# Kernel optimization log

Hardware: AMD Instinct MI355X
Metric: run time of the kernel (lower is better)

## Reference

```python
import jax, jax.numpy as jnp
import numpy as np

D = 192          # d_model
H = 8            # n_heads
DH = D // H      # d_head = 24
DFF = 2 * D      # FeedForward hidden = d_model*2
SIZES = [384 + 8 * i for i in range(32)]   # ragged segment lengths
TOTAL = sum(SIZES)                          # 16256
EPS = 1e-5

# static ragged -> padded index maps (numpy, baked at trace time)
_sz = np.asarray(SIZES)
B = len(_sz)
MAXN = int(_sz.max())
SEG = np.repeat(np.arange(B), _sz)                      # [TOTAL] segment id
POS = np.concatenate([np.arange(s) for s in _sz])       # [TOTAL] position in segment
PADMASK = np.ones((B, MAXN), dtype=bool)                # True = padding (key_padding_mask)
PADMASK[SEG, POS] = False


def _layernorm(x, gamma, beta):
    mu = jnp.mean(x, axis=-1, keepdims=True)
    var = jnp.var(x, axis=-1, keepdims=True)
    return (x - mu) * jax.lax.rsqrt(var + EPS) * gamma + beta


def setup_inputs() -> dict:
    key = jax.random.key(0)
    ks = jax.random.split(key, 8)
    w = lambda k, shape: jax.random.normal(k, shape, jnp.float32) * 0.02
    return {
        "x": jax.random.normal(ks[0], (TOTAL, D), jnp.float32),
        "sizes": jnp.asarray(SIZES, jnp.int32),
        "Wqkv": w(ks[1], (3 * D, D)), "bqkv": jnp.zeros((3 * D,), jnp.float32),
        "Wo": w(ks[2], (D, D)),       "bo": jnp.zeros((D,), jnp.float32),
        "Wg": w(ks[3], (D, 2 * D)),   "bg": jnp.zeros((D,), jnp.float32),
        "gamma1": jnp.ones((D,), jnp.float32), "beta1": jnp.zeros((D,), jnp.float32),
        "W1": w(ks[4], (DFF, D)),     "b1": jnp.zeros((DFF,), jnp.float32),
        "W2": w(ks[5], (D, DFF)),     "b2": jnp.zeros((D,), jnp.float32),
        "gamma2": jnp.ones((D,), jnp.float32), "beta2": jnp.zeros((D,), jnp.float32),
    }


def reference(x, sizes, Wqkv, bqkv, Wo, bo, Wg, bg, gamma1, beta1,
              W1, b1, W2, b2, gamma2, beta2):
    # --- pad_by_sizes (vectorized scatter, static index maps) ---
    pad = jnp.zeros((B, MAXN, D), x.dtype).at[SEG, POS].set(x)   # [B, MAXN, D]

    # --- nn.MultiheadAttention (batch_first, key_padding_mask) ---
    qkv = pad @ Wqkv.T + bqkv                                    # [B, MAXN, 3D]
    q, k, v = jnp.split(qkv, 3, axis=-1)
    def heads(t):  # [B, MAXN, D] -> [B, H, MAXN, DH]
        return t.reshape(B, MAXN, H, DH).transpose(0, 2, 1, 3)
    q, k, v = heads(q), heads(k), heads(v)
    scores = jnp.einsum("bhqd,bhkd->bhqk", q, k) / np.sqrt(DH)   # [B, H, MAXN, MAXN]
    scores = jnp.where(PADMASK[:, None, None, :], jnp.float32(-1e9), scores)
    attn = jax.nn.softmax(scores, axis=-1)
    o = jnp.einsum("bhqk,bhkd->bhqd", attn, v)                   # [B, H, MAXN, DH]
    o = o.transpose(0, 2, 1, 3).reshape(B, MAXN, D)
    out = o @ Wo.T + bo                                          # [B, MAXN, D]

    # --- gather back to ragged; gate/norm/ff are per-token, so the torch
    # per-segment loop is equivalent to one vectorized pass over all tokens ---
    out_flat = out[SEG, POS]                                     # [TOTAL, D]
    g = jax.nn.sigmoid(jnp.concatenate([out_flat, x], axis=-1) @ Wg.T + bg)
    h = g * out_flat + (1.0 - g) * x                             # GatedResidual
    h = _layernorm(h, gamma1, beta1)                             # self.norm
    y = jax.nn.silu(h @ W1.T + b1) @ W2.T + b2                   # FeedForward.net
    return _layernorm(h + y, gamma2, beta2)                      # residual + norm
```

## Files before the change

kernel.cpp:

```cpp
#include <hip/hip_runtime.h>
#include <math.h>

#define D_      192
#define H_      8
#define DH_     24
#define NSEG    32
#define TOTAL_  16256
static constexpr float LN_EPS = 1e-5f;
static constexpr float SCALE  = 0.20412414523193154f;
static constexpr float SC_L2E = 0.29446679331797463f;

typedef float  f32x4  __attribute__((ext_vector_type(4)));
typedef short  bf16x8 __attribute__((ext_vector_type(8)));
typedef unsigned short u16x4 __attribute__((ext_vector_type(4)));
typedef unsigned int   u32x4 __attribute__((ext_vector_type(4)));

__device__ __forceinline__ unsigned short f2b(float f) {
    union { float f; unsigned u; } v; v.f = f;
    unsigned r = v.u + 0x7FFFu + ((v.u >> 16) & 1u);
    return (unsigned short)(r >> 16);
}
__device__ __forceinline__ unsigned f2b_u32(float f) {
    union { float f; unsigned u; } v; v.f = f;
    return (v.u + 0x8000u) >> 16;
}
__device__ __forceinline__ unsigned short f2b_fast(float f) {
    union { float f; unsigned u; } v; v.f = f;
    return (unsigned short)((v.u + 0x8000u) >> 16);
}
__device__ __forceinline__ float b2f(unsigned short h) {
    union { unsigned u; float f; } v; v.u = (unsigned)h << 16; return v.f;
}
__device__ __forceinline__ float fexp2(float x) {
#if __has_builtin(__builtin_amdgcn_exp2f)
    return __builtin_amdgcn_exp2f(x);
#else
    return exp2f(x);
#endif
}

#define NXE 3121152
__global__ __launch_bounds__(256)
void conv_all(const float* __restrict__ x,
              const float* __restrict__ w0, const float* __restrict__ w1,
              const float* __restrict__ w2, const float* __restrict__ w3,
              const float* __restrict__ w4,
              unsigned short* __restrict__ xb, unsigned short* __restrict__ wb)
{
    int i = (blockIdx.x * 256 + threadIdx.x) * 4;
    const float* src; unsigned short* dst; int off;
    if (i < NXE) { src = x; dst = xb; off = 0; }
    else {
        int j = i - NXE; dst = wb;
        if      (j < 110592) { src = w0; off = 0; }
        else if (j < 147456) { src = w1; off = 110592; }
        else if (j < 221184) { src = w2; off = 147456; }
        else if (j < 294912) { src = w3; off = 221184; }
        else                 { src = w4; off = 294912; }
        i = j;
    }
    float4 v = *(const float4*)&src[i - off];
    u16x4 o = { f2b(v.x), f2b(v.y), f2b(v.z), f2b(v.w) };
    *(u16x4*)&dst[i] = o;
}

template<int KF, int MR, int OUT_BF16>
__global__ __launch_bounds__(256)
void gemm_lds(const unsigned short* __restrict__ Ain,
              const unsigned short* __restrict__ Wb,
              const float* __restrict__ bias,
              void* __restrict__ Cout, int N)
{
    constexpr int KSW = KF * 32 + 8;
    __shared__ unsigned short Wp[64 * KSW];

    const int tid = threadIdx.x;
    const int wv  = tid >> 6;
    const int l   = tid & 63;
    const int m0  = blockIdx.x * (64 * MR) + wv * (16 * MR);
    const int n0  = blockIdx.y * 64;
    const int rl  = l & 15;
    const int kc  = (l >> 4) * 8;

    bf16x8 afrag[MR][KF];
    #pragma unroll
    for (int h = 0; h < MR; ++h)
        #pragma unroll
        for (int kk = 0; kk < KF; ++kk)
            afrag[h][kk] = *(const bf16x8*)&Ain[(size_t)(m0 + h * 16 + rl) * (KF * 32) + kk * 32 + kc];

    #pragma unroll
    for (int i = 0; i < KF; ++i) {
        int u = i * 256 + tid;
        int row = u / (KF * 4), c = u % (KF * 4);
        *(bf16x8*)&Wp[row * KSW + c * 8] = *(const bf16x8*)&Wb[(size_t)(n0 + row) * (KF * 32) + c * 8];
    }
    __syncthreads();

    f32x4 acc[MR][4] = {};
    #pragma unroll
    for (int kk = 0; kk < KF; ++kk) {
        #pragma unroll
        for (int nf = 0; nf < 4; ++nf) {
            bf16x8 b = *(const bf16x8*)&Wp[(nf * 16 + rl) * KSW + kk * 32 + kc];
            #pragma unroll
            for (int h = 0; h < MR; ++h)
                acc[h][nf] = __builtin_amdgcn_mfma_f32_16x16x32_bf16(afrag[h][kk], b, acc[h][nf], 0, 0, 0);
        }
    }

    #pragma unroll
    for (int h = 0; h < MR; ++h) {
        #pragma unroll
        for (int nf = 0; nf < 4; ++nf) {
            const int c = n0 + nf * 16 + rl;
            const float bz = bias[c];
            #pragma unroll
            for (int q = 0; q < 4; ++q) {
                const int r = m0 + h * 16 + (l >> 4) * 4 + q;
                float v = acc[h][nf][q] + bz;
                if (OUT_BF16) ((unsigned short*)Cout)[(size_t)r * N + c] = f2b(v);
                else          ((float*)Cout)[(size_t)r * N + c] = v;
            }
        }
    }
}

__global__ __launch_bounds__(256, 2)
void wo_gate_ln1(const unsigned short* __restrict__ o_b,
                 const unsigned short* __restrict__ xb,
                 const unsigned short* __restrict__ wo_b,
                 const unsigned short* __restrict__ wg_b,
                 const float* __restrict__ bo, const float* __restrict__ bg,
                 const float* __restrict__ gamma1, const float* __restrict__ beta1,
                 unsigned short* __restrict__ h1b)
{
    constexpr int WS = 200;
    __shared__ unsigned short Wp[96 * WS];
    __shared__ unsigned short Al[64 * WS];

    const int tid = threadIdx.x;
    const int wv  = tid >> 6;
    const int l   = tid & 63;
    const int rl  = l & 15;
    const int g   = l >> 4;
    const int kc  = g * 8;
    const int m0  = blockIdx.x * 64 + wv * 16;

    bf16x8 afA[6];
    #pragma unroll
    for (int kk = 0; kk < 6; ++kk)
        afA[kk] = *(const bf16x8*)&o_b[(size_t)(m0 + rl) * 192 + kk * 32 + kc];

    f32x4 accA[12] = {};
    #pragma unroll
    for (int sub = 0; sub < 2; ++sub) {
        __syncthreads();
        #pragma unroll
        for (int i = 0; i < 9; ++i) {
            int u = i * 256 + tid;
            int row = u / 24, c = u % 24;
            *(bf16x8*)&Wp[row * WS + c * 8] = *(const bf16x8*)&wo_b[(size_t)(sub * 96 + row) * 192 + c * 8];
        }
        __syncthreads();
        #pragma unroll
        for (int kk = 0; kk < 6; ++kk)
            #pragma unroll
            for (int nf2 = 0; nf2 < 6; ++nf2) {
                bf16x8 b = *(const bf16x8*)&Wp[(nf2 * 16 + rl) * WS + kk * 32 + kc];
                accA[sub * 6 + nf2] = __builtin_amdgcn_mfma_f32_16x16x32_bf16(afA[kk], b, accA[sub * 6 + nf2], 0, 0, 0);
            }
    }

    float att[12][4];
    #pragma unroll
    for (int nf = 0; nf < 12; ++nf) {
        const int cnf = (nf / 6) * 96 + (nf % 6) * 16 + rl;
        const float bz = bo[cnf];
        #pragma unroll
        for (int q = 0; q < 4; ++q) {
            att[nf][q] = accA[nf][q] + bz;
            Al[(wv * 16 + g * 4 + q) * WS + cnf] = f2b(att[nf][q]);
        }
    }

    bf16x8 afX[6];
    #pragma unroll
    for (int kk = 0; kk < 6; ++kk)
        afX[kk] = *(const bf16x8*)&xb[(size_t)(m0 + rl) * 192 + kk * 32 + kc];

    f32x4 accB[12] = {};
    #pragma unroll
    for (int kb = 0; kb < 2; ++kb)
        #pragma unroll
        for (int sub = 0; sub < 2; ++sub) {
            __syncthreads();
            #pragma unroll
            for (int i = 0; i < 9; ++i) {
                int u = i * 256 + tid;
                int row = u / 24, c = u % 24;
                *(bf16x8*)&Wp[row * WS + c * 8] = *(const bf16x8*)&wg_b[(size_t)(sub * 96 + row) * 384 + kb * 192 + c * 8];
            }
            __syncthreads();
            #pragma unroll
            for (int kk = 0; kk < 6; ++kk) {
                bf16x8 a = (kb == 0) ? *(const bf16x8*)&Al[(wv * 16 + rl) * WS + kk * 32 + kc]
                                     : afX[kk];
                #pragma unroll
                for (int nf2 = 0; nf2 < 6; ++nf2) {
                    bf16x8 b = *(const bf16x8*)&Wp[(nf2 * 16 + rl) * WS + kk * 32 + kc];
                    accB[sub * 6 + nf2] = __builtin_amdgcn_mfma_f32_16x16x32_bf16(a, b, accB[sub * 6 + nf2], 0, 0, 0);
                }
            }
        }

    float bz[12], gam[12], bet[12];
    #pragma unroll
    for (int nf = 0; nf < 12; ++nf) {
        const int cnf = (nf / 6) * 96 + (nf % 6) * 16 + rl;
        bz[nf]  = bg[cnf];
        gam[nf] = gamma1[cnf];
        bet[nf] = beta1[cnf];
    }
    #pragma unroll
    for (int q = 0; q < 4; ++q) {
        const int r = m0 + g * 4 + q;
        const size_t rb = (size_t)r * 192;
        float h[12];
        float s = 0.f;
        #pragma unroll
        for (int nf = 0; nf < 12; ++nf) {
            const int cnf = (nf / 6) * 96 + (nf % 6) * 16 + rl;
            float v  = accB[nf][q] + bz[nf];
            float gt = 1.f / (1.f + __expf(-v));
            h[nf] = gt * att[nf][q] + (1.f - gt) * b2f(xb[rb + cnf]);
            s += h[nf];
        }
        s += __shfl_xor(s, 1); s += __shfl_xor(s, 2);
        s += __shfl_xor(s, 4); s += __shfl_xor(s, 8);
        const float mu = s * (1.f / 192.f);
        float sq = 0.f;
        #pragma unroll
        for (int nf = 0; nf < 12; ++nf) { float d = h[nf] - mu; sq += d * d; }
        sq += __shfl_xor(sq, 1); sq += __shfl_xor(sq, 2);
        sq += __shfl_xor(sq, 4); sq += __shfl_xor(sq, 8);
        const float rstd = rsqrtf(sq * (1.f / 192.f) + LN_EPS);
        #pragma unroll
        for (int nf = 0; nf < 12; ++nf) {
            const int cnf = (nf / 6) * 96 + (nf % 6) * 16 + rl;
            h1b[rb + cnf] = f2b((h[nf] - mu) * rstd * gam[nf] + bet[nf]);
        }
    }
}

__global__ __launch_bounds__(256, 2)
void ffn_ln2(const unsigned short* __restrict__ h1b,
             const unsigned short* __restrict__ w1_b,
             const unsigned short* __restrict__ w2_b,
             const float* __restrict__ b1, const float* __restrict__ b2,
             const float* __restrict__ gamma2, const float* __restrict__ beta2,
             float* __restrict__ out)
{
    constexpr int WS = 200;
    __shared__ unsigned short Wp[96 * WS];
    __shared__ unsigned short Fl[64 * WS];

    const int tid = threadIdx.x;
    const int wv  = tid >> 6;
    const int l   = tid & 63;
    const int rl  = l & 15;
    const int g   = l >> 4;
    const int kc  = g * 8;
    const int m0  = blockIdx.x * 64 + wv * 16;

    bf16x8 afC[6];
    #pragma unroll
    for (int kk = 0; kk < 6; ++kk)
        afC[kk] = *(const bf16x8*)&h1b[(size_t)(m0 + rl) * 192 + kk * 32 + kc];

    f32x4 accD[12] = {};
    #pragma unroll
    for (int ch = 0; ch < 2; ++ch) {
        f32x4 accC[12] = {};
        #pragma unroll
        for (int sub = 0; sub < 2; ++sub) {
            __syncthreads();
            #pragma unroll
            for (int i = 0; i < 9; ++i) {
                int u = i * 256 + tid;
                int row = u / 24, c = u % 24;
                *(bf16x8*)&Wp[row * WS + c * 8] = *(const bf16x8*)&w1_b[(size_t)(ch * 192 + sub * 96 + row) * 192 + c * 8];
            }
            __syncthreads();
            #pragma unroll
            for (int kk = 0; kk < 6; ++kk)
                #pragma unroll
                for (int nf2 = 0; nf2 < 6; ++nf2) {
                    bf16x8 b = *(const bf16x8*)&Wp[(nf2 * 16 + rl) * WS + kk * 32 + kc];
                    accC[sub * 6 + nf2] = __builtin_amdgcn_mfma_f32_16x16x32_bf16(afC[kk], b, accC[sub * 6 + nf2], 0, 0, 0);
                }
        }
        #pragma unroll
        for (int nf = 0; nf < 12; ++nf) {
            const int colc = (nf / 6) * 96 + (nf % 6) * 16 + rl;
            const float bz1 = b1[ch * 192 + colc];
            #pragma unroll
            for (int q = 0; q < 4; ++q) {
                float v = accC[nf][q] + bz1;
                float s = 1.f / (1.f + __expf(-v));
                Fl[(wv * 16 + g * 4 + q) * WS + colc] = f2b(v * s);
            }
        }
        #pragma unroll
        for (int sub = 0; sub < 2; ++sub) {
            __syncthreads();
            #pragma unroll
            for (int i = 0; i < 9; ++i) {
                int u = i * 256 + tid;
                int row = u / 24, c = u % 24;
                *(bf16x8*)&Wp[row * WS + c * 8] = *(const bf16x8*)&w2_b[(size_t)(sub * 96 + row) * 384 + ch * 192 + c * 8];
            }
            __syncthreads();
            #pragma unroll
            for (int kk = 0; kk < 6; ++kk) {
                bf16x8 a = *(const bf16x8*)&Fl[(wv * 16 + rl) * WS + kk * 32 + kc];
                #pragma unroll
                for (int nf2 = 0; nf2 < 6; ++nf2) {
                    bf16x8 b = *(const bf16x8*)&Wp[(nf2 * 16 + rl) * WS + kk * 32 + kc];
                    accD[sub * 6 + nf2] = __builtin_amdgcn_mfma_f32_16x16x32_bf16(a, b, accD[sub * 6 + nf2], 0, 0, 0);
                }
            }
        }
    }

    float bz[12], gam[12], bet[12];
    #pragma unroll
    for (int nf = 0; nf < 12; ++nf) {
        const int cnf = (nf / 6) * 96 + (nf % 6) * 16 + rl;
        bz[nf]  = b2[cnf];
        gam[nf] = gamma2[cnf];
        bet[nf] = beta2[cnf];
    }
    #pragma unroll
    for (int q = 0; q < 4; ++q) {
        const int r = m0 + g * 4 + q;
        const size_t rb = (size_t)r * 192;
        float h[12];
        float s = 0.f;
        #pragma unroll
        for (int nf = 0; nf < 12; ++nf) {
            const int cnf = (nf / 6) * 96 + (nf % 6) * 16 + rl;
            h[nf] = b2f(h1b[rb + cnf]) + accD[nf][q] + bz[nf];
            s += h[nf];
        }
        s += __shfl_xor(s, 1); s += __shfl_xor(s, 2);
        s += __shfl_xor(s, 4); s += __shfl_xor(s, 8);
        const float mu = s * (1.f / 192.f);
        float sq = 0.f;
        #pragma unroll
        for (int nf = 0; nf < 12; ++nf) { float d = h[nf] - mu; sq += d * d; }
        sq += __shfl_xor(sq, 1); sq += __shfl_xor(sq, 2);
        sq += __shfl_xor(sq, 4); sq += __shfl_xor(sq, 8);
        const float rstd = rsqrtf(sq * (1.f / 192.f) + LN_EPS);
        #pragma unroll
        for (int nf = 0; nf < 12; ++nf) {
            const int cnf = (nf / 6) * 96 + (nf % 6) * 16 + rl;
            out[rb + cnf] = (h[nf] - mu) * rstd * gam[nf] + bet[nf];
        }
    }
}

#define KSTR 40
#define VSTR 72

__global__ __launch_bounds__(256)
void attn_mfma(const unsigned short* __restrict__ qkv, unsigned short* __restrict__ o)
{
    const int w    = blockIdx.x;
    const int xcd  = w & 7;
    const int slot = w >> 3;
    const int seg  = xcd + 8 * (slot / 40);
    const int inr  = slot % 40;
    const int head = inr / 5;
    const int q0   = (inr % 5) * 128;

    const int n    = 384 + 8 * seg;
    const int base = 384 * seg + 4 * seg * (seg - 1);
    if (q0 >= n) return;

    __shared__ unsigned short Ks[2][64 * KSTR];
    __shared__ unsigned short Vt[2][32 * VSTR];

    const int tid = threadIdx.x;
    const int wv  = tid >> 6;
    const int l   = tid & 63;
    const int lq  = l & 15;
    const int g   = l >> 4;

    if (tid < 64) {
        *(uint4*)&Ks[0][tid * KSTR + 24] = make_uint4(0, 0, 0, 0);
        *(uint4*)&Ks[1][tid * KSTR + 24] = make_uint4(0, 0, 0, 0);
    }
    for (int t4 = tid; t4 < 144; t4 += 256) {
        *(unsigned long long*)&Vt[0][24 * VSTR + t4 * 4] = 0ull;
        *(unsigned long long*)&Vt[1][24 * VSTR + t4 * 4] = 0ull;
    }

    int   qrow[2];
    bf16x8 qfrag[2];
    #pragma unroll
    for (int qf = 0; qf < 2; ++qf) {
        qrow[qf] = q0 + wv * 32 + qf * 16 + lq;
        const int qtok = base + (qrow[qf] < n ? qrow[qf] : n - 1);
        bf16x8 qz = {};
        if (g < 3) qz = *(const bf16x8*)&qkv[(size_t)qtok * 576 + head * 24 + g * 8];
        qfrag[qf] = qz;
    }

    const int sj  = tid & 63;
    const int sc  = tid >> 6;
    const int scj = 32 * (sj >> 5) + 8 * ((sj >> 2) & 3) + 4 * ((sj >> 4) & 1) + (sj & 3);

    bf16x8 kreg = {}, vreg = {};
    if (tid < 192) {
        int jr = sj; if (jr >= n) jr = n - 1;
        const unsigned short* rp = &qkv[(size_t)(base + jr) * 576 + head * 24 + sc * 8];
        kreg = *(const bf16x8*)(rp + 192);
        vreg = *(const bf16x8*)(rp + 384);
        *(bf16x8*)&Ks[0][sj * KSTR + sc * 8] = kreg;
        #pragma unroll
        for (int e = 0; e < 8; ++e)
            Vt[0][(sc * 8 + e) * VSTR + scj] = ((const unsigned short*)&vreg)[e];
    }

    float lsum[2] = {0.f, 0.f};
    f32x4 oacc[2][2] = {};

    const int nt = (n + 63) >> 6;
    int cur = 0;
    for (int t = 0; t < nt; ++t) {
        __syncthreads();
        const int j0 = t * 64;
        const bool pf = (t + 1 < nt) && (tid < 192);
        if (pf) {
            int jr = j0 + 64 + sj; if (jr >= n) jr = n - 1;
            const unsigned short* rp = &qkv[(size_t)(base + jr) * 576 + head * 24 + sc * 8];
            kreg = *(const bf16x8*)(rp + 192);
            vreg = *(const bf16x8*)(rp + 384);
        }

        bf16x8 kf[4];
        #pragma unroll
        for (int ks = 0; ks < 4; ++ks)
            kf[ks] = *(const bf16x8*)&Ks[cur][(ks * 16 + lq) * KSTR + g * 8];

        const int rem = n - j0;
        bf16x8 pfr[2][2];
        #pragma unroll
        for (int qf = 0; qf < 2; ++qf) {
            f32x4 sacc[4] = {};
            #pragma unroll
            for (int ks = 0; ks < 4; ++ks)
                sacc[ks] = __builtin_amdgcn_mfma_f32_16x16x32_bf16(kf[ks], qfrag[qf], sacc[ks], 0, 0, 0);

            float psum = 0.f;
            unsigned pw[8];
            #pragma unroll
            for (int ks = 0; ks < 4; ++ks) {
                float pv[4];
                #pragma unroll
                for (int r = 0; r < 4; ++r) {
                    float p = fexp2(sacc[ks][r] * SC_L2E);
                    if (rem < 64) { int key = ks * 16 + g * 4 + r; if (key >= rem) p = 0.f; }
                    psum += p;
                    pv[r] = p;
                }
                pw[ks * 2 + 0] = f2b_u32(pv[0]) | (f2b_u32(pv[1]) << 16);
                pw[ks * 2 + 1] = f2b_u32(pv[2]) | (f2b_u32(pv[3]) << 16);
            }
            psum += __shfl_xor(psum, 16);
            psum += __shfl_xor(psum, 32);
            lsum[qf] += psum;
            #pragma unroll
            for (int jk = 0; jk < 2; ++jk) {
                u32x4 fr = { pw[jk*4+0], pw[jk*4+1], pw[jk*4+2], pw[jk*4+3] };
                pfr[qf][jk] = *(bf16x8*)&fr;
            }
        }

        #pragma unroll
        for (int jk = 0; jk < 2; ++jk) {
            bf16x8 vf[2];
            #pragma unroll
            for (int df = 0; df < 2; ++df)
                vf[df] = *(const bf16x8*)&Vt[cur][(df * 16 + lq) * VSTR + jk * 32 + g * 8];
            #pragma unroll
            for (int qf = 0; qf < 2; ++qf)
                #pragma unroll
                for (int df = 0; df < 2; ++df)
                    oacc[qf][df] = __builtin_amdgcn_mfma_f32_16x16x32_bf16(vf[df], pfr[qf][jk], oacc[qf][df], 0, 0, 0);
        }

        if (pf) {
            *(bf16x8*)&Ks[cur ^ 1][sj * KSTR + sc * 8] = kreg;
            #pragma unroll
            for (int e = 0; e < 8; ++e)
                Vt[cur ^ 1][(sc * 8 + e) * VSTR + scj] = ((const unsigned short*)&vreg)[e];
        }
        cur ^= 1;
    }

    #pragma unroll
    for (int qf = 0; qf < 2; ++qf) {
        if (qrow[qf] < n) {
            const float rl2 = 1.f / lsum[qf];
            #pragma unroll
            for (int df = 0; df < 2; ++df) {
                const int d0 = df * 16 + g * 4;
                if (d0 < 24) {
                    u16x4 r = { f2b_fast(oacc[qf][df][0] * rl2), f2b_fast(oacc[qf][df][1] * rl2),
                                f2b_fast(oacc[qf][df][2] * rl2), f2b_fast(oacc[qf][df][3] * rl2) };
                    *(u16x4*)&o[(size_t)(base + qrow[qf]) * 192 + head * 24 + d0] = r;
                }
            }
        }
    }
}

extern "C" void kernel_launch(void* const* d_in, const int* in_sizes, int n_in,
                              void* d_out, int out_size, void* d_ws, size_t ws_size,
                              hipStream_t stream)
{
    const float* x      = (const float*)d_in[0];
    const float* Wqkv   = (const float*)d_in[2];
    const float* bqkv   = (const float*)d_in[3];
    const float* Wo     = (const float*)d_in[4];
    const float* bo     = (const float*)d_in[5];
    const float* Wg     = (const float*)d_in[6];
    const float* bg     = (const float*)d_in[7];
    const float* gamma1 = (const float*)d_in[8];
    const float* beta1  = (const float*)d_in[9];
    const float* W1     = (const float*)d_in[10];
    const float* b1     = (const float*)d_in[11];
    const float* W2     = (const float*)d_in[12];
    const float* b2     = (const float*)d_in[13];
    const float* gamma2 = (const float*)d_in[14];
    const float* beta2  = (const float*)d_in[15];
    float* out = (float*)d_out;
    float* ws  = (float*)d_ws;

    const size_t T = TOTAL_;
    unsigned short* qkv_b = (unsigned short*)ws;
    unsigned short* o_b   = (unsigned short*)(ws + 288 * T);
    unsigned short* h1b   = (unsigned short*)(ws + 384 * T);
    unsigned short* wb    = (unsigned short*)(ws + 480 * T);
    unsigned short* xb    = (unsigned short*)(ws + 492 * T);

    dim3 blk(256);

    conv_all<<<dim3(3408), blk, 0, stream>>>(x, Wqkv, Wo, Wg, W1, W2, xb, wb);
    gemm_lds<6,2,1><<<dim3(127, 9), blk, 0, stream>>>(xb, wb, bqkv, qkv_b, 576);
    attn_mfma<<<dim3(1280), blk, 0, stream>>>(qkv_b, o_b);
    wo_gate_ln1<<<dim3(254), blk, 0, stream>>>(o_b, xb, wb + 110592, wb + 147456,
                                               bo, bg, gamma1, beta1, h1b);
    ffn_ln2<<<dim3(254), blk, 0, stream>>>(h1b, wb + 221184, wb + 294912,
                                           b1, b2, gamma2, beta2, out);
}
```

Baseline: 95.90 us.

## Fuse Wo/gate/LN1 and FFN/LN2 kernels into one tail kernel

```diff
diff --git a/kernel.cpp b/kernel.cpp
--- a/kernel.cpp
+++ b/kernel.cpp
@@ -127,13 +127,17 @@
 }
 
 __global__ __launch_bounds__(256, 2)
-void wo_gate_ln1(const unsigned short* __restrict__ o_b,
-                 const unsigned short* __restrict__ xb,
-                 const unsigned short* __restrict__ wo_b,
-                 const unsigned short* __restrict__ wg_b,
-                 const float* __restrict__ bo, const float* __restrict__ bg,
-                 const float* __restrict__ gamma1, const float* __restrict__ beta1,
-                 unsigned short* __restrict__ h1b)
+void tail_fused(const unsigned short* __restrict__ o_b,
+                const unsigned short* __restrict__ xb,
+                const unsigned short* __restrict__ wo_b,
+                const unsigned short* __restrict__ wg_b,
+                const unsigned short* __restrict__ w1_b,
+                const unsigned short* __restrict__ w2_b,
+                const float* __restrict__ bo, const float* __restrict__ bg,
+                const float* __restrict__ b1, const float* __restrict__ b2,
+                const float* __restrict__ gamma1, const float* __restrict__ beta1,
+                const float* __restrict__ gamma2, const float* __restrict__ beta2,
+                float* __restrict__ out)
 {
     constexpr int WS = 200;
     __shared__ unsigned short Wp[96 * WS];
@@ -214,69 +218,58 @@
             }
         }
 
-    float bz[12], gam[12], bet[12];
+    float h1ln[12][4];
+    {
+        float bz[12], gam[12], bet[12];
+        #pragma unroll
+        for (int nf = 0; nf < 12; ++nf) {
+            const int cnf = (nf / 6) * 96 + (nf % 6) * 16 + rl;
+            bz[nf]  = bg[cnf];
+            gam[nf] = gamma1[cnf];
+            bet[nf] = beta1[cnf];
+        }
+        #pragma unroll
+        for (int q = 0; q < 4; ++q) {
+            const int r = m0 + g * 4 + q;
+            const size_t rb = (size_t)r * 192;
+            float h[12];
+            float s = 0.f;
+            #pragma unroll
+            for (int nf = 0; nf < 12; ++nf) {
+                const int cnf = (nf / 6) * 96 + (nf % 6) * 16 + rl;
+                float v  = accB[nf][q] + bz[nf];
+                float gt = 1.f / (1.f + __expf(-v));
+                h[nf] = gt * att[nf][q] + (1.f - gt) * b2f(xb[rb + cnf]);
+                s += h[nf];
+            }
+            s += __shfl_xor(s, 1); s += __shfl_xor(s, 2);
+            s += __shfl_xor(s, 4); s += __shfl_xor(s, 8);
+            const float mu = s * (1.f / 192.f);
+            float sq = 0.f;
+            #pragma unroll
+            for (int nf = 0; nf < 12; ++nf) { float d = h[nf] - mu; sq += d * d; }
+            sq += __shfl_xor(sq, 1); sq += __shfl_xor(sq, 2);
+            sq += __shfl_xor(sq, 4); sq += __shfl_xor(sq, 8);
+            const float rstd = rsqrtf(sq * (1.f / 192.f) + LN_EPS);
+            #pragma unroll
+            for (int nf = 0; nf < 12; ++nf)
+                h1ln[nf][q] = (h[nf] - mu) * rstd * gam[nf] + bet[nf];
+        }
+    }
+    __syncthreads();
     #pragma unroll
     for (int nf = 0; nf < 12; ++nf) {
         const int cnf = (nf / 6) * 96 + (nf % 6) * 16 + rl;
-        bz[nf]  = bg[cnf];
-        gam[nf] = gamma1[cnf];
-        bet[nf] = beta1[cnf];
-    }
-    #pragma unroll
-    for (int q = 0; q < 4; ++q) {
-        const int r = m0 + g * 4 + q;
-        const size_t rb = (size_t)r * 192;
-        float h[12];
-        float s = 0.f;
-        #pragma unroll
-        for (int nf = 0; nf < 12; ++nf) {
-            const int cnf = (nf / 6) * 96 + (nf % 6) * 16 + rl;
-            float v  = accB[nf][q] + bz[nf];
-            float gt = 1.f / (1.f + __expf(-v));
-            h[nf] = gt * att[nf][q] + (1.f - gt) * b2f(xb[rb + cnf]);
-            s += h[nf];
-        }
-        s += __shfl_xor(s, 1); s += __shfl_xor(s, 2);
-        s += __shfl_xor(s, 4); s += __shfl_xor(s, 8);
-        const float mu = s * (1.f / 192.f);
-        float sq = 0.f;
-        #pragma unroll
-        for (int nf = 0; nf < 12; ++nf) { float d = h[nf] - mu; sq += d * d; }
-        sq += __shfl_xor(sq, 1); sq += __shfl_xor(sq, 2);
-        sq += __shfl_xor(sq, 4); sq += __shfl_xor(sq, 8);
-        const float rstd = rsqrtf(sq * (1.f / 192.f) + LN_EPS);
-        #pragma unroll
-        for (int nf = 0; nf < 12; ++nf) {
-            const int cnf = (nf / 6) * 96 + (nf % 6) * 16 + rl;
-            h1b[rb + cnf] = f2b((h[nf] - mu) * rstd * gam[nf] + bet[nf]);
-        }
-    }
-}
-
-__global__ __launch_bounds__(256, 2)
-void ffn_ln2(const unsigned short* __restrict__ h1b,
-             const unsigned short* __restrict__ w1_b,
-             const unsigned short* __restrict__ w2_b,
-             const float* __restrict__ b1, const float* __restrict__ b2,
-             const float* __restrict__ gamma2, const float* __restrict__ beta2,
-             float* __restrict__ out)
-{
-    constexpr int WS = 200;
-    __shared__ unsigned short Wp[96 * WS];
-    __shared__ unsigned short Fl[64 * WS];
-
-    const int tid = threadIdx.x;
-    const int wv  = tid >> 6;
-    const int l   = tid & 63;
-    const int rl  = l & 15;
-    const int g   = l >> 4;
-    const int kc  = g * 8;
-    const int m0  = blockIdx.x * 64 + wv * 16;
+        #pragma unroll
+        for (int q = 0; q < 4; ++q)
+            Al[(wv * 16 + g * 4 + q) * WS + cnf] = f2b(h1ln[nf][q]);
+    }
+    __syncthreads();
 
     bf16x8 afC[6];
     #pragma unroll
     for (int kk = 0; kk < 6; ++kk)
-        afC[kk] = *(const bf16x8*)&h1b[(size_t)(m0 + rl) * 192 + kk * 32 + kc];
+        afC[kk] = *(const bf16x8*)&Al[(wv * 16 + rl) * WS + kk * 32 + kc];
 
     f32x4 accD[12] = {};
     #pragma unroll
@@ -300,6 +293,7 @@
                     accC[sub * 6 + nf2] = __builtin_amdgcn_mfma_f32_16x16x32_bf16(afC[kk], b, accC[sub * 6 + nf2], 0, 0, 0);
                 }
         }
+        __syncthreads();
         #pragma unroll
         for (int nf = 0; nf < 12; ++nf) {
             const int colc = (nf / 6) * 96 + (nf % 6) * 16 + rl;
@@ -308,7 +302,7 @@
             for (int q = 0; q < 4; ++q) {
                 float v = accC[nf][q] + bz1;
                 float s = 1.f / (1.f + __expf(-v));
-                Fl[(wv * 16 + g * 4 + q) * WS + colc] = f2b(v * s);
+                Al[(wv * 16 + g * 4 + q) * WS + colc] = f2b(v * s);
             }
         }
         #pragma unroll
@@ -323,7 +317,7 @@
             __syncthreads();
             #pragma unroll
             for (int kk = 0; kk < 6; ++kk) {
-                bf16x8 a = *(const bf16x8*)&Fl[(wv * 16 + rl) * WS + kk * 32 + kc];
+                bf16x8 a = *(const bf16x8*)&Al[(wv * 16 + rl) * WS + kk * 32 + kc];
                 #pragma unroll
                 for (int nf2 = 0; nf2 < 6; ++nf2) {
                     bf16x8 b = *(const bf16x8*)&Wp[(nf2 * 16 + rl) * WS + kk * 32 + kc];
@@ -349,8 +343,7 @@
         float s = 0.f;
         #pragma unroll
         for (int nf = 0; nf < 12; ++nf) {
-            const int cnf = (nf / 6) * 96 + (nf % 6) * 16 + rl;
-            h[nf] = b2f(h1b[rb + cnf]) + accD[nf][q] + bz[nf];
+            h[nf] = h1ln[nf][q] + accD[nf][q] + bz[nf];
             s += h[nf];
         }
         s += __shfl_xor(s, 1); s += __shfl_xor(s, 2);
@@ -552,17 +545,16 @@
     const size_t T = TOTAL_;
     unsigned short* qkv_b = (unsigned short*)ws;
     unsigned short* o_b   = (unsigned short*)(ws + 288 * T);
-    unsigned short* h1b   = (unsigned short*)(ws + 384 * T);
-    unsigned short* wb    = (unsigned short*)(ws + 480 * T);
-    unsigned short* xb    = (unsigned short*)(ws + 492 * T);
+    unsigned short* wb    = (unsigned short*)(ws + 384 * T);
+    unsigned short* xb    = (unsigned short*)(ws + 396 * T);
 
     dim3 blk(256);
 
     conv_all<<<dim3(3408), blk, 0, stream>>>(x, Wqkv, Wo, Wg, W1, W2, xb, wb);
     gemm_lds<6,2,1><<<dim3(127, 9), blk, 0, stream>>>(xb, wb, bqkv, qkv_b, 576);
     attn_mfma<<<dim3(1280), blk, 0, stream>>>(qkv_b, o_b);
-    wo_gate_ln1<<<dim3(254), blk, 0, stream>>>(o_b, xb, wb + 110592, wb + 147456,
-                                               bo, bg, gamma1, beta1, h1b);
-    ffn_ln2<<<dim3(254), blk, 0, stream>>>(h1b, wb + 221184, wb + 294912,
-                                           b1, b2, gamma2, beta2, out);
-}
+    tail_fused<<<dim3(254), blk, 0, stream>>>(o_b, xb, wb + 110592, wb + 147456,
+                                              wb + 221184, wb + 294912,
+                                              bo, bg, b1, b2,
+                                              gamma1, beta1, gamma2, beta2, out);
+}
```

Measured after the change: 92.75 us. 3.3% less time.
